# Kernel optimization log

Measured on AMD Instinct MI355X. Metric: run time of the kernel, lower is better.

## Reference

```python
import jax, jax.numpy as jnp
import numpy as np
import math

T = 4096          # num tokens (== context_window_len)
IN_SIZE = 2048    # model dim
HEAD_SIZE = 128   # per-head dim


def setup_inputs() -> dict:
    key = jax.random.key(0)
    kx, kq, kk, kv = jax.random.split(key, 4)
    scale = 1.0 / math.sqrt(IN_SIZE)
    x = jax.random.normal(kx, (T, IN_SIZE), dtype=jnp.float32)
    # eqx.nn.Linear(in, out) weight has shape [out, in], applied as W @ x
    Wq = jax.random.normal(kq, (HEAD_SIZE, IN_SIZE), dtype=jnp.float32) * scale
    Wk = jax.random.normal(kk, (HEAD_SIZE, IN_SIZE), dtype=jnp.float32) * scale
    Wv = jax.random.normal(kv, (HEAD_SIZE, IN_SIZE), dtype=jnp.float32) * scale
    return {"x": x, "Wq": Wq, "Wk": Wk, "Wv": Wv}


def reference(x, Wq, Wk, Wv):
    # q, k, v: [T, head_size]
    q = x @ Wq.T
    k = x @ Wk.T
    v = x @ Wv.T
    # scores: [T, T]
    scores = (q @ k.T) / math.sqrt(HEAD_SIZE)
    num_toks = x.shape[0]
    # causal mask: True above the diagonal (masked out)
    causal_mask = ~jnp.tril(jnp.ones((num_toks, num_toks), dtype=bool))
    masked = jnp.where(causal_mask, -jnp.inf, scores)
    attn = jax.nn.softmax(masked, axis=-1)
    return attn @ v
```

## Files before the change

kernel.cpp:

```cpp
#include <hip/hip_runtime.h>
#include <hip/hip_bf16.h>

#define T_TOK 4096
#define D_IN  2048
#define HS    128
#define CKV   4
#define NCH   16

typedef unsigned short u16;
typedef __attribute__((ext_vector_type(8))) __bf16 bf16x8;
typedef __attribute__((ext_vector_type(4))) float f32x4;
typedef __attribute__((ext_vector_type(4))) unsigned short us4;
typedef __attribute__((ext_vector_type(8))) unsigned short us8;

#define GLOBAL_AS __attribute__((address_space(1)))
#define LDS_AS    __attribute__((address_space(3)))

__device__ __forceinline__ void async_ld16(const void* g, void* l) {
  __builtin_amdgcn_global_load_lds((GLOBAL_AS void*)(void*)g, (LDS_AS void*)l, 16, 0, 0);
}

__device__ __forceinline__ u16 f2bf(float v) {
  return __builtin_bit_cast(u16, __float2bfloat16(v));
}

__device__ __forceinline__ bool detect_f32(const u16* in, int tid, int* sflag) {
  if (tid < 64) {
    int cnt = 0;
#pragma unroll
    for (int j = 0; j < 8; j++) {
      u16 v = in[(tid * 8 + j) * 2];
      cnt += (((v >> 7) & 0xFF) >= 0xBF) ? 1 : 0;
    }
#pragma unroll
    for (int off = 1; off < 64; off <<= 1) cnt += __shfl_xor(cnt, off);
    if (tid == 0) *sflag = (cnt > 8) ? 1 : 0;
  }
  __syncthreads();
  return (*sflag != 0);
}

__global__ __launch_bounds__(256) void conv3_kernel(
    const u16* __restrict__ w0, const u16* __restrict__ w1,
    const u16* __restrict__ w2, u16* __restrict__ o0,
    u16* __restrict__ o1, u16* __restrict__ o2, int* __restrict__ flag) {
  __shared__ int sflag;
  const int mat = blockIdx.x >> 7;
  const int blk = blockIdx.x & 127;
  const u16* in = (mat == 0) ? w0 : ((mat == 1) ? w1 : w2);
  u16* out = (mat == 0) ? o0 : ((mat == 1) ? o1 : o2);
  const int tid = threadIdx.x;
  const bool isf32 = detect_f32(in, tid, &sflag);
  if (tid == 0 && mat == 0 && blk == 0) *flag = isf32 ? 1 : 0;
  const size_t base = ((size_t)blk * 256 + tid) * 8;
  if (isf32) {
    const float* f = (const float*)in;
    us4 a, b;
#pragma unroll
    for (int j = 0; j < 4; j++) a[j] = f2bf(f[base + j]);
#pragma unroll
    for (int j = 0; j < 4; j++) b[j] = f2bf(f[base + 4 + j]);
    *(us4*)(out + base) = a;
    *(us4*)(out + base + 4) = b;
  } else {
    *(us8*)(out + base) = *(const us8*)(in + base);
  }
}

__global__ __launch_bounds__(256, 2) void qkv_kernel(
    const u16* __restrict__ x, const u16* __restrict__ Wq,
    const u16* __restrict__ Wk, const u16* __restrict__ Wv,
    u16* __restrict__ Q, u16* __restrict__ K, u16* __restrict__ Vt)
{
  __shared__ __align__(16) u16 As[2][16 * 64];
  __shared__ __align__(16) u16 Bs[2][128 * 64];
  __shared__ int sflag;

  const int mat = blockIdx.y;
  const u16* W = (mat == 0) ? Wq : ((mat == 1) ? Wk : Wv);
  const int mtile = blockIdx.x;
  const int tid = threadIdx.x;
  const int wv = tid >> 6, lane = tid & 63, l15 = lane & 15, quad = lane >> 4;
  const int row0 = mtile * 16;

  const bool isf32 = detect_f32(x, tid, &sflag);

  f32x4 acc[2];
#pragma unroll
  for (int i = 0; i < 2; i++) acc[i] = (f32x4)0.0f;

  const int ar = tid >> 3;
  const int ac = (tid & 7) ^ (ar & 7);

  f32x4 pa[2];
  auto loadA_f32 = [&](int k0) {
    if (tid < 128) {
      const float* xf = (const float*)x + (size_t)(row0 + ar) * D_IN + k0;
      pa[0] = *(const f32x4*)(xf + ac * 8);
      pa[1] = *(const f32x4*)(xf + ac * 8 + 4);
    }
  };
  auto writeA_f32 = [&](int buf) {
    if (tid < 128) {
      us8 c0;
#pragma unroll
      for (int j = 0; j < 4; j++) { c0[j] = f2bf(pa[0][j]); c0[4 + j] = f2bf(pa[1][j]); }
      *(us8*)((char*)As[buf] + (size_t)tid * 16) = c0;
    }
  };
  auto stageA_bf16 = [&](int k0, int buf) {
    if (wv < 2) {
      async_ld16(x + (size_t)(row0 + ar) * D_IN + k0 + ac * 8,
                 (char*)As[buf] + (size_t)wv * 1024);
    }
  };
  auto stageB = [&](int k0, int buf) {
#pragma unroll
    for (int j = 0; j < 4; j++) {
      int s = (wv * 4 + j) * 64 + lane;
      int n = s >> 3, cs = s & 7, c = cs ^ (n & 7);
      async_ld16(W + (size_t)n * D_IN + k0 + c * 8,
                 (char*)Bs[buf] + (size_t)(wv * 4 + j) * 1024);
    }
  };

  stageB(0, 0);
  if (isf32) loadA_f32(0); else stageA_bf16(0, 0);

  for (int kt = 0; kt < 32; kt++) {
    const int cur = kt & 1;
    if (isf32) writeA_f32(cur);
    __syncthreads();
    if (kt < 31) {
      stageB((kt + 1) * 64, 1 - cur);
      if (isf32) loadA_f32((kt + 1) * 64); else stageA_bf16((kt + 1) * 64, 1 - cur);
    }
#pragma unroll
    for (int kc = 0; kc < 2; kc++) {
      const int rA = l15;
      const int cl = kc * 4 + quad;
      bf16x8 a = *(const bf16x8*)((const char*)As[cur] + (rA * 8 + (cl ^ (rA & 7))) * 16);
#pragma unroll
      for (int nt = 0; nt < 2; nt++) {
        int n = wv * 32 + 16 * nt + l15;
        bf16x8 b = *(const bf16x8*)((const char*)Bs[cur] + (n * 8 + (cl ^ (n & 7))) * 16);
        acc[nt] = __builtin_amdgcn_mfma_f32_16x16x32_bf16(a, b, acc[nt], 0, 0, 0);
      }
    }
  }

  if (mat < 2) {
    u16* out = (mat == 0) ? Q : K;
#pragma unroll
    for (int nt = 0; nt < 2; nt++)
#pragma unroll
      for (int r = 0; r < 4; r++) {
        int m = row0 + quad * 4 + r;
        int n = wv * 32 + 16 * nt + l15;
        out[(size_t)m * HS + n] = f2bf(acc[nt][r]);
      }
  } else {
#pragma unroll
    for (int nt = 0; nt < 2; nt++) {
      int n = wv * 32 + 16 * nt + l15;
      int mb = row0 + quad * 4;
      us4 pk;
#pragma unroll
      for (int r = 0; r < 4; r++) pk[r] = f2bf(acc[nt][r]);
      *(us4*)(Vt + (size_t)n * T_TOK + mb) = pk;
    }
  }
}

__global__ __launch_bounds__(256, 2) void attn_split_kernel(
    const u16* __restrict__ Q, const u16* __restrict__ Kg,
    const u16* __restrict__ Vt, float* __restrict__ Opart,
    float* __restrict__ mstat, float* __restrict__ lstat)
{
  __shared__ __align__(16) u16 Ks[2][64 * 128];
  __shared__ __align__(16) u16 Vs[2][128 * 64];
  __shared__ __align__(16) u16 Ps[4 * 16 * 64];

  const int qtile = 63 - (int)blockIdx.x;
  const int ch = blockIdx.y;
  if (4 * ch > qtile) return;
  const int t0 = 4 * ch;
  const int nsteps = min(CKV, qtile + 1 - t0);
  const int q0 = qtile * 64;
  const int slot = 64 * ch - 2 * ch * (ch - 1) + (qtile - 4 * ch);

  const int tid = threadIdx.x;
  const int wv = tid >> 6, lane = tid & 63, l15 = lane & 15, quad = lane >> 4;

  bf16x8 qf[4];
#pragma unroll
  for (int kc = 0; kc < 4; kc++)
    qf[kc] = *(const bf16x8*)(Q + (size_t)(q0 + 16 * wv + l15) * HS + kc * 32 + quad * 8);

  f32x4 o[8];
#pragma unroll
  for (int i = 0; i < 8; i++) o[i] = (f32x4)0.0f;
  float mrun[4], lrun[4];
#pragma unroll
  for (int r = 0; r < 4; r++) { mrun[r] = -1e30f; lrun[r] = 0.0f; }

  const float sc = 0.12752761571239668f;

  auto stage = [&](int t, int buf) {
#pragma unroll
    for (int j = 0; j < 4; j++) {
      int s = (wv * 4 + j) * 64 + lane;
      int n = s >> 4, cs = s & 15, c = cs ^ (n & 7);
      async_ld16(Kg + (size_t)(t * 64 + n) * HS + c * 8,
                 (char*)Ks[buf] + (size_t)(wv * 4 + j) * 1024);
    }
#pragma unroll
    for (int j = 0; j < 4; j++) {
      int s = (wv * 4 + j) * 64 + lane;
      int vr = s >> 3, cs = s & 7, c = cs ^ (vr & 7);
      async_ld16(Vt + (size_t)vr * T_TOK + t * 64 + c * 8,
                 (char*)Vs[buf] + (size_t)(wv * 4 + j) * 1024);
    }
  };

  stage(t0, 0);
  for (int i = 0; i < nsteps; i++) {
    const int cur = i & 1;
    const int t = t0 + i;
    __syncthreads();
    if (i + 1 < nsteps) stage(t + 1, 1 - cur);

    f32x4 sacc[4];
#pragma unroll
    for (int nt = 0; nt < 4; nt++) sacc[nt] = (f32x4)0.0f;
#pragma unroll
    for (int kc = 0; kc < 4; kc++) {
      const int cl = kc * 4 + quad;
#pragma unroll
      for (int nt = 0; nt < 4; nt++) {
        int n = 16 * nt + l15;
        bf16x8 b = *(const bf16x8*)((const char*)Ks[cur] + (n * 16 + (cl ^ (n & 7))) * 16);
        sacc[nt] = __builtin_amdgcn_mfma_f32_16x16x32_bf16(qf[kc], b, sacc[nt], 0, 0, 0);
      }
    }

    float s2[4][4];
    const bool diag = (t == qtile);
#pragma unroll
    for (int nt = 0; nt < 4; nt++)
#pragma unroll
      for (int r = 0; r < 4; r++) {
        float v = sacc[nt][r] * sc;
        if (diag) {
          int qr = q0 + 16 * wv + quad * 4 + r;
          int kr = t * 64 + 16 * nt + l15;
          if (kr > qr) v = -1e30f;
        }
        s2[nt][r] = v;
      }

    float mnew[4], alpha[4];
#pragma unroll
    for (int r = 0; r < 4; r++) {
      float tmax = fmaxf(fmaxf(s2[0][r], s2[1][r]), fmaxf(s2[2][r], s2[3][r]));
#pragma unroll
      for (int off = 1; off < 16; off <<= 1) tmax = fmaxf(tmax, __shfl_xor(tmax, off));
      mnew[r] = fmaxf(mrun[r], tmax);
      alpha[r] = exp2f(mrun[r] - mnew[r]);
      mrun[r] = mnew[r];
    }
    float p[4][4];
#pragma unroll
    for (int r = 0; r < 4; r++) {
      float s = 0.0f;
#pragma unroll
      for (int nt = 0; nt < 4; nt++) { p[nt][r] = exp2f(s2[nt][r] - mnew[r]); s += p[nt][r]; }
#pragma unroll
      for (int off = 1; off < 16; off <<= 1) s += __shfl_xor(s, off);
      lrun[r] = lrun[r] * alpha[r] + s;
    }
#pragma unroll
    for (int c = 0; c < 8; c++)
#pragma unroll
      for (int r = 0; r < 4; r++) o[c][r] *= alpha[r];

    u16* Pw = Ps + wv * 1024;
#pragma unroll
    for (int nt = 0; nt < 4; nt++)
#pragma unroll
      for (int r = 0; r < 4; r++) {
        int row = quad * 4 + r;
        int col = nt * 16 + l15;
        int cc = col >> 3, wi = col & 7;
        Pw[(row * 8 + (cc ^ (row & 7))) * 8 + wi] = f2bf(p[nt][r]);
      }

#pragma unroll
    for (int kc = 0; kc < 2; kc++) {
      const int cl = kc * 4 + quad;
      bf16x8 a = *(const bf16x8*)((const char*)Pw + (l15 * 8 + (cl ^ (l15 & 7))) * 16);
#pragma unroll
      for (int c = 0; c < 8; c++) {
        int vr = 16 * c + l15;
        bf16x8 b = *(const bf16x8*)((const char*)Vs[cur] + (vr * 8 + (cl ^ (vr & 7))) * 16);
        o[c] = __builtin_amdgcn_mfma_f32_16x16x32_bf16(a, b, o[c], 0, 0, 0);
      }
    }
  }

  float* po = Opart + (size_t)slot * 64 * 128;
#pragma unroll
  for (int c = 0; c < 8; c++)
#pragma unroll
    for (int r = 0; r < 4; r++) {
      int ml = 16 * wv + quad * 4 + r;
      po[ml * 128 + 16 * c + l15] = o[c][r];
    }
  if (l15 == 0) {
#pragma unroll
    for (int r = 0; r < 4; r++) {
      int ml = 16 * wv + quad * 4 + r;
      mstat[slot * 64 + ml] = mrun[r];
      lstat[slot * 64 + ml] = lrun[r];
    }
  }
}

__global__ __launch_bounds__(256) void combine_kernel(
    const float* __restrict__ Opart, const float* __restrict__ mstat,
    const float* __restrict__ lstat, void* __restrict__ out_v,
    const int* __restrict__ dflag)
{
  const int q = blockIdx.x;
  const int cb = blockIdx.y;
  const int tid = threadIdx.x;
  const int row = tid >> 2;
  const int col = cb * 32 + (tid & 3) * 8;
  const int nch = (q + 4) / 4;
  const bool of32 = (*dflag != 0);

  float M = -1e30f;
  {
    int base = 0;
    for (int c = 0; c < nch; c++) {
      int s = base + q - 4 * c;
      M = fmaxf(M, mstat[s * 64 + row]);
      base += 64 - 4 * c;
    }
  }
  float l = 0.0f;
  float acc[8];
#pragma unroll
  for (int j = 0; j < 8; j++) acc[j] = 0.0f;
  {
    int base = 0;
    for (int c = 0; c < nch; c++) {
      int s = base + q - 4 * c;
      float w = exp2f(mstat[s * 64 + row] - M);
      l += w * lstat[s * 64 + row];
      const float* op = Opart + ((size_t)s * 64 + row) * 128 + col;
      f32x4 a = *(const f32x4*)op;
      f32x4 b = *(const f32x4*)(op + 4);
#pragma unroll
      for (int j = 0; j < 4; j++) { acc[j] += w * a[j]; acc[4 + j] += w * b[j]; }
      base += 64 - 4 * c;
    }
  }
  const float inv = 1.0f / l;
  const size_t goff = (size_t)(q * 64 + row) * HS + col;
  if (of32) {
    float* out = (float*)out_v + goff;
    f32x4 r0, r1;
#pragma unroll
    for (int j = 0; j < 4; j++) { r0[j] = acc[j] * inv; r1[j] = acc[4 + j] * inv; }
    *(f32x4*)out = r0;
    *(f32x4*)(out + 4) = r1;
  } else {
    u16* out = (u16*)out_v + goff;
    us4 r0, r1;
#pragma unroll
    for (int j = 0; j < 4; j++) { r0[j] = f2bf(acc[j] * inv); r1[j] = f2bf(acc[4 + j] * inv); }
    *(us4*)out = r0;
    *(us4*)(out + 4) = r1;
  }
}

extern "C" void kernel_launch(void* const* d_in, const int* in_sizes, int n_in,
                              void* d_out, int out_size, void* d_ws, size_t ws_size,
                              hipStream_t stream) {
  const u16* x  = (const u16*)d_in[0];
  const u16* Wq = (const u16*)d_in[1];
  const u16* Wk = (const u16*)d_in[2];
  const u16* Wv = (const u16*)d_in[3];

  float* Opart = (float*)d_ws;
  float* mstat = Opart + (size_t)544 * 64 * 128;
  float* lstat = mstat + (size_t)544 * 64;

  u16* Wqb = (u16*)(lstat + (size_t)544 * 64);
  u16* Wkb = Wqb + (size_t)HS * D_IN;
  u16* Wvb = Wkb + (size_t)HS * D_IN;
  u16* Q   = Wvb + (size_t)HS * D_IN;
  u16* K   = Q   + (size_t)T_TOK * HS;
  u16* Vt  = K   + (size_t)T_TOK * HS;
  int* flag = (int*)(Vt + (size_t)T_TOK * HS);

  conv3_kernel<<<384, 256, 0, stream>>>(Wq, Wk, Wv, Wqb, Wkb, Wvb, flag);
  qkv_kernel<<<dim3(256, 3), 256, 0, stream>>>(x, Wqb, Wkb, Wvb, Q, K, Vt);
  attn_split_kernel<<<dim3(64, NCH), 256, 0, stream>>>(Q, K, Vt, Opart, mstat, lstat);
  combine_kernel<<<dim3(64, 4), 256, 0, stream>>>(Opart, mstat, lstat, d_out, flag);
}
```

Baseline: 138.3 us.

## Pre-convert x to bf16, enlarge QKV M-tile, triple-buffer loads, add setprio

The conversion kernel now also converts x from fp32 to bf16 into a workspace buffer. This lets the QKV GEMM stage A through async global-to-LDS loads instead of register loads plus conversion. The QKV kernel doubles its M tile to 32 rows (half the blocks) and moves to a 3-stage LDS pipeline that waits with explicit vmcnt and raw s_barrier. MFMA sections in both QKV and attention are wrapped in s_setprio. The cost is an extra pass over x through memory, plus larger LDS use that may reduce occupancy.

```diff
diff --git a/kernel.cpp b/kernel.cpp
--- a/kernel.cpp
+++ b/kernel.cpp
@@ -40,135 +40,148 @@
   return (*sflag != 0);
 }
 
-__global__ __launch_bounds__(256) void conv3_kernel(
+__global__ __launch_bounds__(256) void cvt_kernel(
     const u16* __restrict__ w0, const u16* __restrict__ w1,
-    const u16* __restrict__ w2, u16* __restrict__ o0,
-    u16* __restrict__ o1, u16* __restrict__ o2, int* __restrict__ flag) {
+    const u16* __restrict__ w2, const u16* __restrict__ x,
+    u16* __restrict__ o0, u16* __restrict__ o1, u16* __restrict__ o2,
+    u16* __restrict__ xb, int* __restrict__ flag) {
   __shared__ int sflag;
-  const int mat = blockIdx.x >> 7;
-  const int blk = blockIdx.x & 127;
-  const u16* in = (mat == 0) ? w0 : ((mat == 1) ? w1 : w2);
-  u16* out = (mat == 0) ? o0 : ((mat == 1) ? o1 : o2);
+  const int b = blockIdx.x;
   const int tid = threadIdx.x;
-  const bool isf32 = detect_f32(in, tid, &sflag);
-  if (tid == 0 && mat == 0 && blk == 0) *flag = isf32 ? 1 : 0;
-  const size_t base = ((size_t)blk * 256 + tid) * 8;
-  if (isf32) {
-    const float* f = (const float*)in;
-    us4 a, b;
+  if (b < 384) {
+    const int mat = b >> 7;
+    const int blk = b & 127;
+    const u16* in = (mat == 0) ? w0 : ((mat == 1) ? w1 : w2);
+    u16* out = (mat == 0) ? o0 : ((mat == 1) ? o1 : o2);
+    const bool isf32 = detect_f32(in, tid, &sflag);
+    if (tid == 0 && b == 0) *flag = isf32 ? 1 : 0;
+    const size_t base = ((size_t)blk * 256 + tid) * 8;
+    if (isf32) {
+      const float* f = (const float*)in;
+      us4 a, c;
+#pragma unroll
+      for (int j = 0; j < 4; j++) a[j] = f2bf(f[base + j]);
+#pragma unroll
+      for (int j = 0; j < 4; j++) c[j] = f2bf(f[base + 4 + j]);
+      *(us4*)(out + base) = a;
+      *(us4*)(out + base + 4) = c;
+    } else {
+      *(us8*)(out + base) = *(const us8*)(in + base);
+    }
+  } else {
+    const bool isf32 = detect_f32(x, tid, &sflag);
+    if (!isf32) return;
+    const int blk = b - 384;
+    const size_t base = ((size_t)blk * 256 + tid) * 8;
+    const float* f = (const float*)x;
+    us4 a, c;
 #pragma unroll
     for (int j = 0; j < 4; j++) a[j] = f2bf(f[base + j]);
 #pragma unroll
-    for (int j = 0; j < 4; j++) b[j] = f2bf(f[base + 4 + j]);
-    *(us4*)(out + base) = a;
-    *(us4*)(out + base + 4) = b;
-  } else {
-    *(us8*)(out + base) = *(const us8*)(in + base);
+    for (int j = 0; j < 4; j++) c[j] = f2bf(f[base + 4 + j]);
+    *(us4*)(xb + base) = a;
+    *(us4*)(xb + base + 4) = c;
   }
 }
 
 __global__ __launch_bounds__(256, 2) void qkv_kernel(
-    const u16* __restrict__ x, const u16* __restrict__ Wq,
-    const u16* __restrict__ Wk, const u16* __restrict__ Wv,
+    const u16* __restrict__ x, const u16* __restrict__ xb,
+    const u16* __restrict__ Wq, const u16* __restrict__ Wk,
+    const u16* __restrict__ Wv,
     u16* __restrict__ Q, u16* __restrict__ K, u16* __restrict__ Vt)
 {
-  __shared__ __align__(16) u16 As[2][16 * 64];
-  __shared__ __align__(16) u16 Bs[2][128 * 64];
+  __shared__ __align__(16) u16 As[3][32 * 64];
+  __shared__ __align__(16) u16 Bs[3][128 * 64];
   __shared__ int sflag;
 
   const int mat = blockIdx.y;
   const u16* W = (mat == 0) ? Wq : ((mat == 1) ? Wk : Wv);
-  const int mtile = blockIdx.x;
+  const int row0 = blockIdx.x * 32;
   const int tid = threadIdx.x;
   const int wv = tid >> 6, lane = tid & 63, l15 = lane & 15, quad = lane >> 4;
-  const int row0 = mtile * 16;
 
   const bool isf32 = detect_f32(x, tid, &sflag);
-
-  f32x4 acc[2];
-#pragma unroll
-  for (int i = 0; i < 2; i++) acc[i] = (f32x4)0.0f;
-
-  const int ar = tid >> 3;
-  const int ac = (tid & 7) ^ (ar & 7);
-
-  f32x4 pa[2];
-  auto loadA_f32 = [&](int k0) {
-    if (tid < 128) {
-      const float* xf = (const float*)x + (size_t)(row0 + ar) * D_IN + k0;
-      pa[0] = *(const f32x4*)(xf + ac * 8);
-      pa[1] = *(const f32x4*)(xf + ac * 8 + 4);
+  const u16* A = isf32 ? xb : x;
+
+  f32x4 acc[2][2];
+#pragma unroll
+  for (int i = 0; i < 2; i++)
+#pragma unroll
+    for (int j = 0; j < 2; j++) acc[i][j] = (f32x4)0.0f;
+
+  auto stage = [&](int k0, int buf) {
+    {
+      int id = wv * 64 + lane;
+      int r = id >> 3, c = (id & 7) ^ (r & 7);
+      async_ld16(A + (size_t)(row0 + r) * D_IN + k0 + c * 8,
+                 (char*)As[buf] + (size_t)wv * 1024);
+    }
+#pragma unroll
+    for (int j = 0; j < 4; j++) {
+      int id = j * 256 + wv * 64 + lane;
+      int n = id >> 3, c = (id & 7) ^ (n & 7);
+      async_ld16(W + (size_t)n * D_IN + k0 + c * 8,
+                 (char*)Bs[buf] + (size_t)j * 4096 + (size_t)wv * 1024);
     }
   };
-  auto writeA_f32 = [&](int buf) {
-    if (tid < 128) {
-      us8 c0;
-#pragma unroll
-      for (int j = 0; j < 4; j++) { c0[j] = f2bf(pa[0][j]); c0[4 + j] = f2bf(pa[1][j]); }
-      *(us8*)((char*)As[buf] + (size_t)tid * 16) = c0;
-    }
-  };
-  auto stageA_bf16 = [&](int k0, int buf) {
-    if (wv < 2) {
-      async_ld16(x + (size_t)(row0 + ar) * D_IN + k0 + ac * 8,
-                 (char*)As[buf] + (size_t)wv * 1024);
-    }
-  };
-  auto stageB = [&](int k0, int buf) {
-#pragma unroll
-    for (int j = 0; j < 4; j++) {
-      int s = (wv * 4 + j) * 64 + lane;
-      int n = s >> 3, cs = s & 7, c = cs ^ (n & 7);
-      async_ld16(W + (size_t)n * D_IN + k0 + c * 8,
-                 (char*)Bs[buf] + (size_t)(wv * 4 + j) * 1024);
-    }
-  };
-
-  stageB(0, 0);
-  if (isf32) loadA_f32(0); else stageA_bf16(0, 0);
+
+  stage(0, 0);
+  stage(64, 1);
 
   for (int kt = 0; kt < 32; kt++) {
-    const int cur = kt & 1;
-    if (isf32) writeA_f32(cur);
-    __syncthreads();
+    const int cur = kt % 3;
     if (kt < 31) {
-      stageB((kt + 1) * 64, 1 - cur);
-      if (isf32) loadA_f32((kt + 1) * 64); else stageA_bf16((kt + 1) * 64, 1 - cur);
-    }
+      asm volatile("s_waitcnt vmcnt(5) lgkmcnt(0)" ::: "memory");
+    } else {
+      asm volatile("s_waitcnt vmcnt(0) lgkmcnt(0)" ::: "memory");
+    }
+    __builtin_amdgcn_s_barrier();
+    __builtin_amdgcn_sched_barrier(0);
+    if (kt + 2 < 32) stage((kt + 2) * 64, (kt + 2) % 3);
+
+    __builtin_amdgcn_s_setprio(1);
 #pragma unroll
     for (int kc = 0; kc < 2; kc++) {
-      const int rA = l15;
       const int cl = kc * 4 + quad;
-      bf16x8 a = *(const bf16x8*)((const char*)As[cur] + (rA * 8 + (cl ^ (rA & 7))) * 16);
-#pragma unroll
-      for (int nt = 0; nt < 2; nt++) {
-        int n = wv * 32 + 16 * nt + l15;
-        bf16x8 b = *(const bf16x8*)((const char*)Bs[cur] + (n * 8 + (cl ^ (n & 7))) * 16);
-        acc[nt] = __builtin_amdgcn_mfma_f32_16x16x32_bf16(a, b, acc[nt], 0, 0, 0);
-      }
-    }
+#pragma unroll
+      for (int mi = 0; mi < 2; mi++) {
+        const int rA = mi * 16 + l15;
+        bf16x8 a = *(const bf16x8*)((const char*)As[cur] + (rA * 8 + (cl ^ (rA & 7))) * 16);
+#pragma unroll
+        for (int nt = 0; nt < 2; nt++) {
+          const int n = wv * 32 + nt * 16 + l15;
+          bf16x8 b = *(const bf16x8*)((const char*)Bs[cur] + (n * 8 + (cl ^ (n & 7))) * 16);
+          acc[mi][nt] = __builtin_amdgcn_mfma_f32_16x16x32_bf16(a, b, acc[mi][nt], 0, 0, 0);
+        }
+      }
+    }
+    __builtin_amdgcn_s_setprio(0);
   }
 
   if (mat < 2) {
     u16* out = (mat == 0) ? Q : K;
 #pragma unroll
-    for (int nt = 0; nt < 2; nt++)
-#pragma unroll
-      for (int r = 0; r < 4; r++) {
-        int m = row0 + quad * 4 + r;
-        int n = wv * 32 + 16 * nt + l15;
-        out[(size_t)m * HS + n] = f2bf(acc[nt][r]);
-      }
+    for (int mi = 0; mi < 2; mi++)
+#pragma unroll
+      for (int nt = 0; nt < 2; nt++)
+#pragma unroll
+        for (int r = 0; r < 4; r++) {
+          int m = row0 + mi * 16 + quad * 4 + r;
+          int n = wv * 32 + nt * 16 + l15;
+          out[(size_t)m * HS + n] = f2bf(acc[mi][nt][r]);
+        }
   } else {
 #pragma unroll
-    for (int nt = 0; nt < 2; nt++) {
-      int n = wv * 32 + 16 * nt + l15;
-      int mb = row0 + quad * 4;
-      us4 pk;
-#pragma unroll
-      for (int r = 0; r < 4; r++) pk[r] = f2bf(acc[nt][r]);
-      *(us4*)(Vt + (size_t)n * T_TOK + mb) = pk;
-    }
+    for (int mi = 0; mi < 2; mi++)
+#pragma unroll
+      for (int nt = 0; nt < 2; nt++) {
+        int n = wv * 32 + nt * 16 + l15;
+        int mb = row0 + mi * 16 + quad * 4;
+        us4 pk;
+#pragma unroll
+        for (int r = 0; r < 4; r++) pk[r] = f2bf(acc[mi][nt][r]);
+        *(us4*)(Vt + (size_t)n * T_TOK + mb) = pk;
+      }
   }
 }
 
@@ -233,6 +246,7 @@
     f32x4 sacc[4];
 #pragma unroll
     for (int nt = 0; nt < 4; nt++) sacc[nt] = (f32x4)0.0f;
+    __builtin_amdgcn_s_setprio(1);
 #pragma unroll
     for (int kc = 0; kc < 4; kc++) {
       const int cl = kc * 4 + quad;
@@ -243,6 +257,7 @@
         sacc[nt] = __builtin_amdgcn_mfma_f32_16x16x32_bf16(qf[kc], b, sacc[nt], 0, 0, 0);
       }
     }
+    __builtin_amdgcn_s_setprio(0);
 
     float s2[4][4];
     const bool diag = (t == qtile);
@@ -295,6 +310,7 @@
         Pw[(row * 8 + (cc ^ (row & 7))) * 8 + wi] = f2bf(p[nt][r]);
       }
 
+    __builtin_amdgcn_s_setprio(1);
 #pragma unroll
     for (int kc = 0; kc < 2; kc++) {
       const int cl = kc * 4 + quad;
@@ -306,6 +322,7 @@
         o[c] = __builtin_amdgcn_mfma_f32_16x16x32_bf16(a, b, o[c], 0, 0, 0);
       }
     }
+    __builtin_amdgcn_s_setprio(0);
   }
 
   float* po = Opart + (size_t)slot * 64 * 128;
@@ -404,9 +421,10 @@
   u16* K   = Q   + (size_t)T_TOK * HS;
   u16* Vt  = K   + (size_t)T_TOK * HS;
   int* flag = (int*)(Vt + (size_t)T_TOK * HS);
-
-  conv3_kernel<<<384, 256, 0, stream>>>(Wq, Wk, Wv, Wqb, Wkb, Wvb, flag);
-  qkv_kernel<<<dim3(256, 3), 256, 0, stream>>>(x, Wqb, Wkb, Wvb, Q, K, Vt);
+  u16* xb  = (u16*)((char*)flag + 16);
+
+  cvt_kernel<<<4480, 256, 0, stream>>>(Wq, Wk, Wv, x, Wqb, Wkb, Wvb, xb, flag);
+  qkv_kernel<<<dim3(128, 3), 256, 0, stream>>>(x, xb, Wqb, Wkb, Wvb, Q, K, Vt);
   attn_split_kernel<<<dim3(64, NCH), 256, 0, stream>>>(Q, K, Vt, Opart, mstat, lstat);
   combine_kernel<<<dim3(64, 4), 256, 0, stream>>>(Opart, mstat, lstat, d_out, flag);
 }
```

Result: slower. 143.9 us (+4.0%).

## Fuse split-KV combine into attention via last-block atomic counter, lazy rescale

Applied to the files above, without the earlier changes.

Removes the separate combine kernel launch: each attention block bumps a per-query-tile atomic counter, and the last-arriving block merges the partial outputs and writes the final result. The online softmax now rescales only when the running max grows by more than a threshold, which skips most alpha multiplies. s_setprio is raised around the MFMA loops. In exchange, the final merge for a tile is serialized inside one block at the tail, and the workspace counter must be reset each call, which conv3 now does.

```diff
diff --git a/kernel.cpp b/kernel.cpp
--- a/kernel.cpp
+++ b/kernel.cpp
@@ -43,7 +43,8 @@
 __global__ __launch_bounds__(256) void conv3_kernel(
     const u16* __restrict__ w0, const u16* __restrict__ w1,
     const u16* __restrict__ w2, u16* __restrict__ o0,
-    u16* __restrict__ o1, u16* __restrict__ o2, int* __restrict__ flag) {
+    u16* __restrict__ o1, u16* __restrict__ o2, int* __restrict__ flag,
+    int* __restrict__ cnt) {
   __shared__ int sflag;
   const int mat = blockIdx.x >> 7;
   const int blk = blockIdx.x & 127;
@@ -51,7 +52,10 @@
   u16* out = (mat == 0) ? o0 : ((mat == 1) ? o1 : o2);
   const int tid = threadIdx.x;
   const bool isf32 = detect_f32(in, tid, &sflag);
-  if (tid == 0 && mat == 0 && blk == 0) *flag = isf32 ? 1 : 0;
+  if (mat == 0 && blk == 0) {
+    if (tid == 0) *flag = isf32 ? 1 : 0;
+    if (tid < 64) cnt[tid] = 0;
+  }
   const size_t base = ((size_t)blk * 256 + tid) * 8;
   if (isf32) {
     const float* f = (const float*)in;
@@ -175,11 +179,14 @@
 __global__ __launch_bounds__(256, 2) void attn_split_kernel(
     const u16* __restrict__ Q, const u16* __restrict__ Kg,
     const u16* __restrict__ Vt, float* __restrict__ Opart,
-    float* __restrict__ mstat, float* __restrict__ lstat)
+    float* __restrict__ mstat, float* __restrict__ lstat,
+    void* __restrict__ out_v, const int* __restrict__ dflag,
+    int* __restrict__ cnt)
 {
   __shared__ __align__(16) u16 Ks[2][64 * 128];
   __shared__ __align__(16) u16 Vs[2][128 * 64];
   __shared__ __align__(16) u16 Ps[4 * 16 * 64];
+  __shared__ int slast;
 
   const int qtile = 63 - (int)blockIdx.x;
   const int ch = blockIdx.y;
@@ -233,6 +240,7 @@
     f32x4 sacc[4];
 #pragma unroll
     for (int nt = 0; nt < 4; nt++) sacc[nt] = (f32x4)0.0f;
+    __builtin_amdgcn_s_setprio(1);
 #pragma unroll
     for (int kc = 0; kc < 4; kc++) {
       const int cl = kc * 4 + quad;
@@ -243,6 +251,7 @@
         sacc[nt] = __builtin_amdgcn_mfma_f32_16x16x32_bf16(qf[kc], b, sacc[nt], 0, 0, 0);
       }
     }
+    __builtin_amdgcn_s_setprio(0);
 
     float s2[4][4];
     const bool diag = (t == qtile);
@@ -259,30 +268,29 @@
         s2[nt][r] = v;
       }
 
-    float mnew[4], alpha[4];
 #pragma unroll
     for (int r = 0; r < 4; r++) {
       float tmax = fmaxf(fmaxf(s2[0][r], s2[1][r]), fmaxf(s2[2][r], s2[3][r]));
 #pragma unroll
       for (int off = 1; off < 16; off <<= 1) tmax = fmaxf(tmax, __shfl_xor(tmax, off));
-      mnew[r] = fmaxf(mrun[r], tmax);
-      alpha[r] = exp2f(mrun[r] - mnew[r]);
-      mrun[r] = mnew[r];
+      if (tmax > mrun[r] + 8.0f) {
+        float alpha = exp2f(mrun[r] - tmax);
+#pragma unroll
+        for (int c = 0; c < 8; c++) o[c][r] *= alpha;
+        lrun[r] *= alpha;
+        mrun[r] = tmax;
+      }
     }
     float p[4][4];
 #pragma unroll
     for (int r = 0; r < 4; r++) {
       float s = 0.0f;
 #pragma unroll
-      for (int nt = 0; nt < 4; nt++) { p[nt][r] = exp2f(s2[nt][r] - mnew[r]); s += p[nt][r]; }
+      for (int nt = 0; nt < 4; nt++) { p[nt][r] = exp2f(s2[nt][r] - mrun[r]); s += p[nt][r]; }
 #pragma unroll
       for (int off = 1; off < 16; off <<= 1) s += __shfl_xor(s, off);
-      lrun[r] = lrun[r] * alpha[r] + s;
-    }
-#pragma unroll
-    for (int c = 0; c < 8; c++)
-#pragma unroll
-      for (int r = 0; r < 4; r++) o[c][r] *= alpha[r];
+      lrun[r] += s;
+    }
 
     u16* Pw = Ps + wv * 1024;
 #pragma unroll
@@ -295,6 +303,7 @@
         Pw[(row * 8 + (cc ^ (row & 7))) * 8 + wi] = f2bf(p[nt][r]);
       }
 
+    __builtin_amdgcn_s_setprio(1);
 #pragma unroll
     for (int kc = 0; kc < 2; kc++) {
       const int cl = kc * 4 + quad;
@@ -306,6 +315,7 @@
         o[c] = __builtin_amdgcn_mfma_f32_16x16x32_bf16(a, b, o[c], 0, 0, 0);
       }
     }
+    __builtin_amdgcn_s_setprio(0);
   }
 
   float* po = Opart + (size_t)slot * 64 * 128;
@@ -324,64 +334,68 @@
       lstat[slot * 64 + ml] = lrun[r];
     }
   }
-}
-
-__global__ __launch_bounds__(256) void combine_kernel(
-    const float* __restrict__ Opart, const float* __restrict__ mstat,
-    const float* __restrict__ lstat, void* __restrict__ out_v,
-    const int* __restrict__ dflag)
-{
-  const int q = blockIdx.x;
-  const int cb = blockIdx.y;
-  const int tid = threadIdx.x;
+
+  const int nchq = qtile / 4 + 1;
+  __threadfence();
+  __syncthreads();
+  if (tid == 0) {
+    int prev = __hip_atomic_fetch_add(cnt + qtile, 1, __ATOMIC_ACQ_REL,
+                                      __HIP_MEMORY_SCOPE_AGENT);
+    slast = (prev == nchq - 1) ? 1 : 0;
+  }
+  __syncthreads();
+  if (slast == 0) return;
+  __threadfence();
+
+  const bool of32 = (*dflag != 0);
   const int row = tid >> 2;
-  const int col = cb * 32 + (tid & 3) * 8;
-  const int nch = (q + 4) / 4;
-  const bool of32 = (*dflag != 0);
-
-  float M = -1e30f;
-  {
-    int base = 0;
-    for (int c = 0; c < nch; c++) {
-      int s = base + q - 4 * c;
-      M = fmaxf(M, mstat[s * 64 + row]);
-      base += 64 - 4 * c;
-    }
-  }
-  float l = 0.0f;
-  float acc[8];
-#pragma unroll
-  for (int j = 0; j < 8; j++) acc[j] = 0.0f;
-  {
-    int base = 0;
-    for (int c = 0; c < nch; c++) {
-      int s = base + q - 4 * c;
-      float w = exp2f(mstat[s * 64 + row] - M);
-      l += w * lstat[s * 64 + row];
-      const float* op = Opart + ((size_t)s * 64 + row) * 128 + col;
-      f32x4 a = *(const f32x4*)op;
-      f32x4 b = *(const f32x4*)(op + 4);
-#pragma unroll
-      for (int j = 0; j < 4; j++) { acc[j] += w * a[j]; acc[4 + j] += w * b[j]; }
-      base += 64 - 4 * c;
-    }
-  }
-  const float inv = 1.0f / l;
-  const size_t goff = (size_t)(q * 64 + row) * HS + col;
-  if (of32) {
-    float* out = (float*)out_v + goff;
-    f32x4 r0, r1;
-#pragma unroll
-    for (int j = 0; j < 4; j++) { r0[j] = acc[j] * inv; r1[j] = acc[4 + j] * inv; }
-    *(f32x4*)out = r0;
-    *(f32x4*)(out + 4) = r1;
-  } else {
-    u16* out = (u16*)out_v + goff;
-    us4 r0, r1;
-#pragma unroll
-    for (int j = 0; j < 4; j++) { r0[j] = f2bf(acc[j] * inv); r1[j] = f2bf(acc[4 + j] * inv); }
-    *(us4*)out = r0;
-    *(us4*)(out + 4) = r1;
+#pragma unroll
+  for (int cb = 0; cb < 4; cb++) {
+    const int col = cb * 32 + (tid & 3) * 8;
+    float M = -1e30f;
+    {
+      int base = 0;
+      for (int c = 0; c < nchq; c++) {
+        int sl = base + qtile - 4 * c;
+        M = fmaxf(M, mstat[sl * 64 + row]);
+        base += 64 - 4 * c;
+      }
+    }
+    float l = 0.0f;
+    float acc[8];
+#pragma unroll
+    for (int j = 0; j < 8; j++) acc[j] = 0.0f;
+    {
+      int base = 0;
+      for (int c = 0; c < nchq; c++) {
+        int sl = base + qtile - 4 * c;
+        float w = exp2f(mstat[sl * 64 + row] - M);
+        l += w * lstat[sl * 64 + row];
+        const float* op = Opart + ((size_t)sl * 64 + row) * 128 + col;
+        f32x4 a = *(const f32x4*)op;
+        f32x4 b = *(const f32x4*)(op + 4);
+#pragma unroll
+        for (int j = 0; j < 4; j++) { acc[j] += w * a[j]; acc[4 + j] += w * b[j]; }
+        base += 64 - 4 * c;
+      }
+    }
+    const float inv = 1.0f / l;
+    const size_t goff = (size_t)(q0 + row) * HS + col;
+    if (of32) {
+      float* out = (float*)out_v + goff;
+      f32x4 r0, r1;
+#pragma unroll
+      for (int j = 0; j < 4; j++) { r0[j] = acc[j] * inv; r1[j] = acc[4 + j] * inv; }
+      *(f32x4*)out = r0;
+      *(f32x4*)(out + 4) = r1;
+    } else {
+      u16* out = (u16*)out_v + goff;
+      us4 r0, r1;
+#pragma unroll
+      for (int j = 0; j < 4; j++) { r0[j] = f2bf(acc[j] * inv); r1[j] = f2bf(acc[4 + j] * inv); }
+      *(us4*)out = r0;
+      *(us4*)(out + 4) = r1;
+    }
   }
 }
 
@@ -404,9 +418,10 @@
   u16* K   = Q   + (size_t)T_TOK * HS;
   u16* Vt  = K   + (size_t)T_TOK * HS;
   int* flag = (int*)(Vt + (size_t)T_TOK * HS);
-
-  conv3_kernel<<<384, 256, 0, stream>>>(Wq, Wk, Wv, Wqb, Wkb, Wvb, flag);
+  int* cnt  = flag + 16;
+
+  conv3_kernel<<<384, 256, 0, stream>>>(Wq, Wk, Wv, Wqb, Wkb, Wvb, flag, cnt);
   qkv_kernel<<<dim3(256, 3), 256, 0, stream>>>(x, Wqb, Wkb, Wvb, Q, K, Vt);
-  attn_split_kernel<<<dim3(64, NCH), 256, 0, stream>>>(Q, K, Vt, Opart, mstat, lstat);
-  combine_kernel<<<dim3(64, 4), 256, 0, stream>>>(Opart, mstat, lstat, d_out, flag);
-}
+  attn_split_kernel<<<dim3(64, NCH), 256, 0, stream>>>(
+      Q, K, Vt, Opart, mstat, lstat, d_out, flag, cnt);
+}
```

New measurement: 251.3 us. 1.82x slower.
